# Optimization experiments

Measured on AMD Instinct MI355X. Metric: run time of the kernel, lower is better.

## Reference

```python
import jax, jax.numpy as jnp
import numpy as np

B, T, D, H, O = 128, 1024, 256, 512, 256

def setup_inputs() -> dict:
    key = jax.random.key(0)
    k0, k1, k2, k3 = jax.random.split(key, 4)
    s_i = 1.0 / np.sqrt(D)
    s_h = 1.0 / np.sqrt(H)
    return {
        "X": jax.random.normal(k0, (B, T, D), jnp.float32),
        "Wi": jax.random.normal(k1, (D, 4 * H), jnp.float32) * s_i,  # input kernel (no bias in flax OptimizedLSTMCell input dense)
        "Wh": jax.random.normal(k2, (H, 4 * H), jnp.float32) * s_h,  # recurrent kernel
        "b": jnp.zeros((4 * H,), jnp.float32),                        # recurrent bias
        "Wd": jax.random.normal(k3, (H, O), jnp.float32) * s_h,      # output Dense kernel
        "bd": jnp.zeros((O,), jnp.float32),                           # output Dense bias
    }

def _lstm_last_hidden(X, Wi, Wh, b):
    # Precompute input projections for all timesteps (same linear map, hoisted out of scan)
    x_proj = jnp.einsum('btd,dg->btg', X, Wi)  # [B, T, 4H]
    h_dim = Wh.shape[0]
    c0 = jnp.zeros((X.shape[0], h_dim), X.dtype)
    h0 = c0

    def step(carry, xt):
        c, h = carry
        y = xt + h @ Wh + b  # [B, 4H]
        i, f, g, o = jnp.split(y, 4, axis=-1)  # flax OptimizedLSTMCell gate order: i, f, g, o
        i = jax.nn.sigmoid(i)
        f = jax.nn.sigmoid(f)
        g = jnp.tanh(g)
        o = jax.nn.sigmoid(o)
        c_new = f * c + i * g
        h_new = o * jnp.tanh(c_new)
        return (c_new, h_new), None

    (c_T, h_T), _ = jax.lax.scan(step, (c0, h0), jnp.swapaxes(x_proj, 0, 1))
    return h_T  # [B, H] = last hidden state

def reference(X, Wi, Wh, b, Wd, bd):
    # Original applies Dense to all timesteps then slices [:, -1, :];
    # Dense is pointwise over time, so applying it to the last hidden is identical math.
    h_last = _lstm_last_hidden(X, Wi, Wh, b)
    return h_last @ Wd + bd  # [B, O]
```

## Files before the change

kernel.cpp:

```cpp
#include <hip/hip_runtime.h>
#include <hip/hip_bf16.h>

#define Bb 128
#define Tt 1024
#define Dd 256
#define Hh 512
#define G4 2048
#define Oo 256

#define NBG 8
#define WPB 8
#define NWG 64
#define BLOCK 512

#define SPIN_CAP (1u << 22)

typedef __attribute__((ext_vector_type(8)))  short  short8;
typedef __attribute__((ext_vector_type(4)))  float  f32x4;
typedef unsigned long long u64;

#define XCC_OFF  0
#define CNT_OFF  256
#define HBUF_OFF 4096
#define WS_ZERO_BYTES (4096 + Bb*Hh*2)

__device__ __forceinline__ short f2bf(float f) {
  __hip_bfloat16 h = __float2bfloat16(f);
  return *reinterpret_cast<short*>(&h);
}
__device__ __forceinline__ float sigm(float x) {
  return __builtin_amdgcn_rcpf(1.f + __expf(-x));
}
__device__ __forceinline__ float tanh_(float x) {
  return fmaf(2.f, __builtin_amdgcn_rcpf(1.f + __expf(-2.f * x)), -1.f);
}

__global__ __launch_bounds__(BLOCK, 2) void lstm_seq(
    const float* __restrict__ X, const float* __restrict__ Wi,
    const float* __restrict__ Wh, const float* __restrict__ bias,
    char* hbuf, int* cnts, int* xcc_post)
{
  __shared__ char sH[16 * 1024];
  __shared__ char sX[16 * 512];
  __shared__ float sY[8][16][36];
  __shared__ unsigned short hstage[16][72];
  __shared__ int sFast;

  const int tid  = threadIdx.x;
  const int w    = tid >> 6;
  const int lane = tid & 63;

  const int bg  = blockIdx.x & 7;
  const int gjw = blockIdx.x >> 3;

  int myxcc;
  asm volatile("s_getreg_b32 %0, hwreg(HW_REG_XCC_ID)" : "=s"(myxcc));
  if (tid == 0) {
    __hip_atomic_store(&xcc_post[blockIdx.x], myxcc + 1,
                       __ATOMIC_RELAXED, __HIP_MEMORY_SCOPE_AGENT);
    int ok = 1;
    for (int p = 0; p < WPB; ++p) {
      int v; unsigned spin = 0;
      do {
        v = __hip_atomic_load(&xcc_post[bg + p * NBG],
                              __ATOMIC_RELAXED, __HIP_MEMORY_SCOPE_AGENT);
      } while (v == 0 && ++spin < SPIN_CAP);
      ok &= (v == myxcc + 1);
    }
    sFast = ok;
  }
  __syncthreads();
  const bool fast = (sFast != 0);
  int* cnt = cnts + bg * 32;

  short8 wf[2][24];
  float bv[2];
#pragma unroll
  for (int nt = 0; nt < 2; ++nt) {
    int c = nt * 16 + (lane & 15);
    int gate = c >> 3, jj = c & 7;
    int colg = gate * Hh + gjw * 64 + w * 8 + jj;
    bv[nt] = bias[colg];
#pragma unroll
    for (int kk = 0; kk < 24; ++kk) {
      short8 f;
#pragma unroll
      for (int i = 0; i < 8; ++i) {
        int k = kk * 32 + (lane >> 4) * 8 + i;
        float v = (k < Hh) ? Wh[(size_t)k * G4 + colg]
                           : Wi[(size_t)(k - Hh) * G4 + colg];
        f[i] = f2bf(v);
      }
      wf[nt][kk] = f;
    }
  }

  const int ejj = lane & 7;
  const int er0 = lane >> 3;
  float cpr[2] = {0.f, 0.f};

  const int arow = lane & 15;
  const int kgrp = lane >> 4;
  const int aswz = (arow & 7) << 4;

  for (int s = 1; s <= Tt; ++s) {
    const char* hread  = hbuf + (size_t)((s - 1) & 1) * (Bb * Hh * 2);
    char*       hwrite = hbuf + (size_t)(s & 1) * (Bb * Hh * 2);

    {
      int row = tid >> 5, seg = tid & 31;
      const float* xp = X + ((size_t)(bg * 16 + row) * Tt + (s - 1)) * Dd + seg * 8;
      f32x4 x0 = *reinterpret_cast<const f32x4*>(xp);
      f32x4 x1 = *reinterpret_cast<const f32x4*>(xp + 4);
      short8 xb;
      xb[0] = f2bf(x0[0]); xb[1] = f2bf(x0[1]); xb[2] = f2bf(x0[2]); xb[3] = f2bf(x0[3]);
      xb[4] = f2bf(x1[0]); xb[5] = f2bf(x1[1]); xb[6] = f2bf(x1[2]); xb[7] = f2bf(x1[3]);
      *reinterpret_cast<short8*>(sX + row * 512 + ((seg * 16) ^ ((row & 7) << 4))) = xb;
    }

    if (s > 1 && tid == 0) {
      const int tgt = WPB * (s - 1);
      unsigned spin = 0;
      if (fast) {
        while ((__hip_atomic_fetch_add(cnt, 0x10000, __ATOMIC_RELAXED,
                                       __HIP_MEMORY_SCOPE_WORKGROUP) & 0xFFFF) < tgt
               && ++spin < SPIN_CAP) {
          __builtin_amdgcn_s_sleep(1);
        }
      } else {
        while (__hip_atomic_load(cnt, __ATOMIC_RELAXED,
                                 __HIP_MEMORY_SCOPE_AGENT) < tgt
               && ++spin < SPIN_CAP) {
          __builtin_amdgcn_s_sleep(1);
        }
      }
    }
    __syncthreads();

    if (fast) {
      asm volatile("buffer_inv sc0" ::: "memory");
#pragma unroll
      for (int q = 0; q < 2; ++q) {
        int c = tid + q * 512, row = c >> 6, off = c & 63;
        f32x4 v = *reinterpret_cast<const f32x4*>(
            hread + (size_t)(bg * 16 + row) * 1024 + off * 16);
        *reinterpret_cast<f32x4*>(sH + row * 1024 + ((off * 16) ^ ((row & 7) << 4))) = v;
      }
    } else {
#pragma unroll
      for (int q = 0; q < 2; ++q) {
        int c = tid + q * 512, row = c >> 6, off = c & 63;
        const u64* src = reinterpret_cast<const u64*>(
            hread + (size_t)(bg * 16 + row) * 1024 + off * 16);
        u64 lo = __hip_atomic_load(src,     __ATOMIC_RELAXED, __HIP_MEMORY_SCOPE_AGENT);
        u64 hi = __hip_atomic_load(src + 1, __ATOMIC_RELAXED, __HIP_MEMORY_SCOPE_AGENT);
        union { u64 u[2]; f32x4 v; } cv; cv.u[0] = lo; cv.u[1] = hi;
        *reinterpret_cast<f32x4*>(sH + row * 1024 + ((off * 16) ^ ((row & 7) << 4))) = cv.v;
      }
    }
    __syncthreads();

    f32x4 acc0, acc1;
#pragma unroll
    for (int m = 0; m < 4; ++m) { acc0[m] = bv[0]; acc1[m] = bv[1]; }
#pragma unroll
    for (int kk = 0; kk < 16; ++kk) {
      short8 a = *reinterpret_cast<const short8*>(
          sH + arow * 1024 + ((kk * 64 + kgrp * 16) ^ aswz));
      acc0 = __builtin_amdgcn_mfma_f32_16x16x32_bf16(a, wf[0][kk], acc0, 0, 0, 0);
      acc1 = __builtin_amdgcn_mfma_f32_16x16x32_bf16(a, wf[1][kk], acc1, 0, 0, 0);
    }
#pragma unroll
    for (int kk = 0; kk < 8; ++kk) {
      short8 a = *reinterpret_cast<const short8*>(
          sX + arow * 512 + ((kk * 64 + kgrp * 16) ^ aswz));
      acc0 = __builtin_amdgcn_mfma_f32_16x16x32_bf16(a, wf[0][16 + kk], acc0, 0, 0, 0);
      acc1 = __builtin_amdgcn_mfma_f32_16x16x32_bf16(a, wf[1][16 + kk], acc1, 0, 0, 0);
    }

    float* sYw = &sY[w][0][0];
#pragma unroll
    for (int m = 0; m < 4; ++m) {
      int row = kgrp * 4 + m;
      sYw[row * 36 + (lane & 15)]      = acc0[m];
      sYw[row * 36 + 16 + (lane & 15)] = acc1[m];
    }
#pragma unroll
    for (int q = 0; q < 2; ++q) {
      int r = er0 + q * 8;
      float yi = sYw[r * 36 + ejj];
      float yf = sYw[r * 36 + 8 + ejj];
      float yg = sYw[r * 36 + 16 + ejj];
      float yo = sYw[r * 36 + 24 + ejj];
      float ig = sigm(yi), fg = sigm(yf), gg = tanh_(yg), og = sigm(yo);
      float c = fg * cpr[q] + ig * gg;
      cpr[q] = c;
      float hh = og * tanh_(c);
      __hip_bfloat16 hb = __float2bfloat16(hh);
      hstage[r][w * 8 + ejj] = *reinterpret_cast<unsigned short*>(&hb);
    }
    __syncthreads();

    if (tid < 128) {
      int row = tid >> 3, colq = tid & 7;
      f32x4 v = *reinterpret_cast<const f32x4*>(
          reinterpret_cast<const char*>(&hstage[0][0]) + row * 144 + colq * 16);
      char* dst = hwrite + ((size_t)(bg * 16 + row) * Hh + gjw * 64 + colq * 8) * 2;
      if (fast) {
        *reinterpret_cast<f32x4*>(dst) = v;
      } else {
        union { f32x4 v; u64 u[2]; } cv; cv.v = v;
        u64* d64 = reinterpret_cast<u64*>(dst);
        __hip_atomic_store(d64,     cv.u[0], __ATOMIC_RELAXED, __HIP_MEMORY_SCOPE_AGENT);
        __hip_atomic_store(d64 + 1, cv.u[1], __ATOMIC_RELAXED, __HIP_MEMORY_SCOPE_AGENT);
      }
    }
    __syncthreads();

    if (tid == 0) {
      if (fast) (void)__hip_atomic_fetch_add(cnt, 1, __ATOMIC_RELAXED,
                                             __HIP_MEMORY_SCOPE_WORKGROUP);
      else      (void)__hip_atomic_fetch_add(cnt, 1, __ATOMIC_RELAXED,
                                             __HIP_MEMORY_SCOPE_AGENT);
    }
  }
}

__global__ void out_dense(const __hip_bfloat16* __restrict__ hT,
                          const float* __restrict__ Wd,
                          const float* __restrict__ bd,
                          float* __restrict__ out)
{
  __shared__ float hrow[Hh];
  int b = blockIdx.x;
  int o = threadIdx.x;
  for (int k = o; k < Hh; k += Oo)
    hrow[k] = __bfloat162float(hT[(size_t)b * Hh + k]);
  __syncthreads();
  float acc = bd[o];
  for (int k = 0; k < Hh; ++k)
    acc = fmaf(hrow[k], Wd[(size_t)k * Oo + o], acc);
  out[(size_t)b * Oo + o] = acc;
}

extern "C" void kernel_launch(void* const* d_in, const int* in_sizes, int n_in,
                              void* d_out, int out_size, void* d_ws, size_t ws_size,
                              hipStream_t stream) {
  (void)in_sizes; (void)n_in; (void)out_size; (void)ws_size;
  const float* X  = (const float*)d_in[0];
  const float* Wi = (const float*)d_in[1];
  const float* Wh = (const float*)d_in[2];
  const float* b  = (const float*)d_in[3];
  const float* Wd = (const float*)d_in[4];
  const float* bd = (const float*)d_in[5];
  float* out = (float*)d_out;

  char* ws = (char*)d_ws;
  int* xcc_post = (int*)(ws + XCC_OFF);
  int* cnts     = (int*)(ws + CNT_OFF);
  char* hbuf    = ws + HBUF_OFF;

  hipMemsetAsync(d_ws, 0, WS_ZERO_BYTES, stream);
  lstm_seq<<<NWG, BLOCK, 0, stream>>>(X, Wi, Wh, b, hbuf, cnts, xcc_post);
  out_dense<<<Bb, Oo, 0, stream>>>((const __hip_bfloat16*)hbuf, Wd, bd, out);
}
```

Measured before the change: 2.751 ms.

## Restructure LSTM step: direct global h loads, shuffle gate exchange, prefetch X, fewer barriers

Reworks the per-timestep schedule of the persistent LSTM kernel. X for the next steps is prefetched into registers two steps ahead, and its MFMA contribution is computed before the inter-block wait. On the fast path, h is loaded straight from global memory into MFMA operands instead of being staged through LDS. Gate values are exchanged with lane shuffles rather than an LDS round trip. h is written directly to global memory, and __syncthreads is replaced by raw s_barrier with explicit waitcnts. The spin-wait sleep is also removed. The changes aim to cut barriers and LDS traffic on the serial critical path, at the cost of uncoalesced 2-byte global stores and fragile manual memory ordering.

Result: slower. 8.194 ms (+197.8%).

```diff
diff --git a/kernel.cpp b/kernel.cpp
--- a/kernel.cpp
+++ b/kernel.cpp
@@ -34,6 +34,21 @@
 __device__ __forceinline__ float tanh_(float x) {
   return fmaf(2.f, __builtin_amdgcn_rcpf(1.f + __expf(-2.f * x)), -1.f);
 }
+
+__device__ __forceinline__ void bar_ctrl() {
+  asm volatile("s_barrier" ::: "memory");
+}
+__device__ __forceinline__ void bar_lds() {
+  asm volatile("s_waitcnt lgkmcnt(0)\n\ts_barrier" ::: "memory");
+}
+__device__ __forceinline__ void bar_vm2() {
+  asm volatile("s_waitcnt vmcnt(2) lgkmcnt(0)\n\ts_barrier" ::: "memory");
+}
+__device__ __forceinline__ void bar_vm0() {
+  asm volatile("s_waitcnt vmcnt(0) lgkmcnt(0)\n\ts_barrier" ::: "memory");
+}
+
+#define MFMA16(A, B, C) __builtin_amdgcn_mfma_f32_16x16x32_bf16((A), (B), (C), 0, 0, 0)
 
 __global__ __launch_bounds__(BLOCK, 2) void lstm_seq(
     const float* __restrict__ X, const float* __restrict__ Wi,
@@ -42,8 +57,6 @@
 {
   __shared__ char sH[16 * 1024];
   __shared__ char sX[16 * 512];
-  __shared__ float sY[8][16][36];
-  __shared__ unsigned short hstage[16][72];
   __shared__ int sFast;
 
   const int tid  = threadIdx.x;
@@ -78,8 +91,8 @@
 #pragma unroll
   for (int nt = 0; nt < 2; ++nt) {
     int c = nt * 16 + (lane & 15);
-    int gate = c >> 3, jj = c & 7;
-    int colg = gate * Hh + gjw * 64 + w * 8 + jj;
+    int gate = c >> 3, jj0 = c & 7;
+    int colg = gate * Hh + gjw * 64 + w * 8 + jj0;
     bv[nt] = bias[colg];
 #pragma unroll
     for (int kk = 0; kk < 24; ++kk) {
@@ -95,27 +108,43 @@
     }
   }
 
-  const int ejj = lane & 7;
-  const int er0 = lane >> 3;
+  const int cjj  = lane & 15;
+  const int kgrp = lane >> 4;
+  const int arow = cjj;
+  const int aswz = (arow & 7) << 4;
+  const int hi8  = (cjj >> 3) & 1;
+  const int jj   = cjj & 7;
+  const int ocol = gjw * 64 + w * 8 + jj;
   float cpr[2] = {0.f, 0.f};
 
-  const int arow = lane & 15;
-  const int kgrp = lane >> 4;
-  const int aswz = (arow & 7) << 4;
-
-  for (int s = 1; s <= Tt; ++s) {
-    const char* hread  = hbuf + (size_t)((s - 1) & 1) * (Bb * Hh * 2);
-    char*       hwrite = hbuf + (size_t)(s & 1) * (Bb * Hh * 2);
+  const int xrow = tid >> 5, xseg = tid & 31;
+  const float* xbase = X + (size_t)(bg * 16 + xrow) * Tt * Dd + xseg * 8;
+  f32x4 xA0 = *reinterpret_cast<const f32x4*>(xbase);
+  f32x4 xA1 = *reinterpret_cast<const f32x4*>(xbase + 4);
+  f32x4 xB0 = *reinterpret_cast<const f32x4*>(xbase + Dd);
+  f32x4 xB1 = *reinterpret_cast<const f32x4*>(xbase + Dd + 4);
+
+  auto STEP = [&](int s, f32x4& xv0, f32x4& xv1) {
+    const char* hread = hbuf + (size_t)((s - 1) & 1) * (Bb * Hh * 2);
+    char*      hwrite = hbuf + (size_t)(s & 1) * (Bb * Hh * 2);
 
     {
-      int row = tid >> 5, seg = tid & 31;
-      const float* xp = X + ((size_t)(bg * 16 + row) * Tt + (s - 1)) * Dd + seg * 8;
-      f32x4 x0 = *reinterpret_cast<const f32x4*>(xp);
-      f32x4 x1 = *reinterpret_cast<const f32x4*>(xp + 4);
       short8 xb;
-      xb[0] = f2bf(x0[0]); xb[1] = f2bf(x0[1]); xb[2] = f2bf(x0[2]); xb[3] = f2bf(x0[3]);
-      xb[4] = f2bf(x1[0]); xb[5] = f2bf(x1[1]); xb[6] = f2bf(x1[2]); xb[7] = f2bf(x1[3]);
-      *reinterpret_cast<short8*>(sX + row * 512 + ((seg * 16) ^ ((row & 7) << 4))) = xb;
+      xb[0] = f2bf(xv0[0]); xb[1] = f2bf(xv0[1]); xb[2] = f2bf(xv0[2]); xb[3] = f2bf(xv0[3]);
+      xb[4] = f2bf(xv1[0]); xb[5] = f2bf(xv1[1]); xb[6] = f2bf(xv1[2]); xb[7] = f2bf(xv1[3]);
+      *reinterpret_cast<short8*>(sX + xrow * 512 + ((xseg * 16) ^ ((xrow & 7) << 4))) = xb;
+    }
+    bar_lds();
+
+    f32x4 acc0, acc1;
+#pragma unroll
+    for (int m = 0; m < 4; ++m) { acc0[m] = bv[0]; acc1[m] = bv[1]; }
+#pragma unroll
+    for (int kk = 0; kk < 8; ++kk) {
+      short8 a = *reinterpret_cast<const short8*>(
+          sX + arow * 512 + ((kk * 64 + kgrp * 16) ^ aswz));
+      acc0 = MFMA16(a, wf[0][16 + kk], acc0);
+      acc1 = MFMA16(a, wf[1][16 + kk], acc1);
     }
 
     if (s > 1 && tid == 0) {
@@ -124,9 +153,7 @@
       if (fast) {
         while ((__hip_atomic_fetch_add(cnt, 0x10000, __ATOMIC_RELAXED,
                                        __HIP_MEMORY_SCOPE_WORKGROUP) & 0xFFFF) < tgt
-               && ++spin < SPIN_CAP) {
-          __builtin_amdgcn_s_sleep(1);
-        }
+               && ++spin < SPIN_CAP) {}
       } else {
         while (__hip_atomic_load(cnt, __ATOMIC_RELAXED,
                                  __HIP_MEMORY_SCOPE_AGENT) < tgt
@@ -135,17 +162,44 @@
         }
       }
     }
-    __syncthreads();
+    bar_ctrl();
 
     if (fast) {
       asm volatile("buffer_inv sc0" ::: "memory");
-#pragma unroll
-      for (int q = 0; q < 2; ++q) {
-        int c = tid + q * 512, row = c >> 6, off = c & 63;
-        f32x4 v = *reinterpret_cast<const f32x4*>(
-            hread + (size_t)(bg * 16 + row) * 1024 + off * 16);
-        *reinterpret_cast<f32x4*>(sH + row * 1024 + ((off * 16) ^ ((row & 7) << 4))) = v;
-      }
+      const char* hb = hread + (size_t)(bg * 16 + arow) * (Hh * 2) + kgrp * 16;
+      short8 a0, a1, a2, a3, b0, b1, b2, b3;
+      a0 = *reinterpret_cast<const short8*>(hb + 0 * 64);
+      a1 = *reinterpret_cast<const short8*>(hb + 1 * 64);
+      a2 = *reinterpret_cast<const short8*>(hb + 2 * 64);
+      a3 = *reinterpret_cast<const short8*>(hb + 3 * 64);
+      b0 = *reinterpret_cast<const short8*>(hb + 4 * 64);
+      b1 = *reinterpret_cast<const short8*>(hb + 5 * 64);
+      b2 = *reinterpret_cast<const short8*>(hb + 6 * 64);
+      b3 = *reinterpret_cast<const short8*>(hb + 7 * 64);
+      acc0 = MFMA16(a0, wf[0][0], acc0); acc1 = MFMA16(a0, wf[1][0], acc1);
+      acc0 = MFMA16(a1, wf[0][1], acc0); acc1 = MFMA16(a1, wf[1][1], acc1);
+      acc0 = MFMA16(a2, wf[0][2], acc0); acc1 = MFMA16(a2, wf[1][2], acc1);
+      acc0 = MFMA16(a3, wf[0][3], acc0); acc1 = MFMA16(a3, wf[1][3], acc1);
+      a0 = *reinterpret_cast<const short8*>(hb + 8 * 64);
+      a1 = *reinterpret_cast<const short8*>(hb + 9 * 64);
+      a2 = *reinterpret_cast<const short8*>(hb + 10 * 64);
+      a3 = *reinterpret_cast<const short8*>(hb + 11 * 64);
+      acc0 = MFMA16(b0, wf[0][4], acc0); acc1 = MFMA16(b0, wf[1][4], acc1);
+      acc0 = MFMA16(b1, wf[0][5], acc0); acc1 = MFMA16(b1, wf[1][5], acc1);
+      acc0 = MFMA16(b2, wf[0][6], acc0); acc1 = MFMA16(b2, wf[1][6], acc1);
+      acc0 = MFMA16(b3, wf[0][7], acc0); acc1 = MFMA16(b3, wf[1][7], acc1);
+      b0 = *reinterpret_cast<const short8*>(hb + 12 * 64);
+      b1 = *reinterpret_cast<const short8*>(hb + 13 * 64);
+      b2 = *reinterpret_cast<const short8*>(hb + 14 * 64);
+      b3 = *reinterpret_cast<const short8*>(hb + 15 * 64);
+      acc0 = MFMA16(a0, wf[0][8],  acc0); acc1 = MFMA16(a0, wf[1][8],  acc1);
+      acc0 = MFMA16(a1, wf[0][9],  acc0); acc1 = MFMA16(a1, wf[1][9],  acc1);
+      acc0 = MFMA16(a2, wf[0][10], acc0); acc1 = MFMA16(a2, wf[1][10], acc1);
+      acc0 = MFMA16(a3, wf[0][11], acc0); acc1 = MFMA16(a3, wf[1][11], acc1);
+      acc0 = MFMA16(b0, wf[0][12], acc0); acc1 = MFMA16(b0, wf[1][12], acc1);
+      acc0 = MFMA16(b1, wf[0][13], acc0); acc1 = MFMA16(b1, wf[1][13], acc1);
+      acc0 = MFMA16(b2, wf[0][14], acc0); acc1 = MFMA16(b2, wf[1][14], acc1);
+      acc0 = MFMA16(b3, wf[0][15], acc0); acc1 = MFMA16(b3, wf[1][15], acc1);
     } else {
 #pragma unroll
       for (int q = 0; q < 2; ++q) {
@@ -157,65 +211,67 @@
         union { u64 u[2]; f32x4 v; } cv; cv.u[0] = lo; cv.u[1] = hi;
         *reinterpret_cast<f32x4*>(sH + row * 1024 + ((off * 16) ^ ((row & 7) << 4))) = cv.v;
       }
-    }
-    __syncthreads();
-
-    f32x4 acc0, acc1;
-#pragma unroll
-    for (int m = 0; m < 4; ++m) { acc0[m] = bv[0]; acc1[m] = bv[1]; }
-#pragma unroll
-    for (int kk = 0; kk < 16; ++kk) {
-      short8 a = *reinterpret_cast<const short8*>(
-          sH + arow * 1024 + ((kk * 64 + kgrp * 16) ^ aswz));
-      acc0 = __builtin_amdgcn_mfma_f32_16x16x32_bf16(a, wf[0][kk], acc0, 0, 0, 0);
-      acc1 = __builtin_amdgcn_mfma_f32_16x16x32_bf16(a, wf[1][kk], acc1, 0, 0, 0);
-    }
-#pragma unroll
-    for (int kk = 0; kk < 8; ++kk) {
-      short8 a = *reinterpret_cast<const short8*>(
-          sX + arow * 512 + ((kk * 64 + kgrp * 16) ^ aswz));
-      acc0 = __builtin_amdgcn_mfma_f32_16x16x32_bf16(a, wf[0][16 + kk], acc0, 0, 0, 0);
-      acc1 = __builtin_amdgcn_mfma_f32_16x16x32_bf16(a, wf[1][16 + kk], acc1, 0, 0, 0);
-    }
-
-    float* sYw = &sY[w][0][0];
+      bar_lds();
+#pragma unroll
+      for (int kk = 0; kk < 16; ++kk) {
+        short8 a = *reinterpret_cast<const short8*>(
+            sH + arow * 1024 + ((kk * 64 + kgrp * 16) ^ aswz));
+        acc0 = MFMA16(a, wf[0][kk], acc0);
+        acc1 = MFMA16(a, wf[1][kk], acc1);
+      }
+    }
+
+    float o0[4], o1[4];
 #pragma unroll
     for (int m = 0; m < 4; ++m) {
-      int row = kgrp * 4 + m;
-      sYw[row * 36 + (lane & 15)]      = acc0[m];
-      sYw[row * 36 + 16 + (lane & 15)] = acc1[m];
-    }
+      o0[m] = __shfl_xor(acc0[m], 8);
+      o1[m] = __shfl_xor(acc1[m], 8);
+    }
+    float hv[2];
 #pragma unroll
     for (int q = 0; q < 2; ++q) {
-      int r = er0 + q * 8;
-      float yi = sYw[r * 36 + ejj];
-      float yf = sYw[r * 36 + 8 + ejj];
-      float yg = sYw[r * 36 + 16 + ejj];
-      float yo = sYw[r * 36 + 24 + ejj];
-      float ig = sigm(yi), fg = sigm(yf), gg = tanh_(yg), og = sigm(yo);
+      int m = hi8 * 2 + q;
+      float iv = hi8 ? o0[m]   : acc0[m];
+      float fv = hi8 ? acc0[m] : o0[m];
+      float gv = hi8 ? o1[m]   : acc1[m];
+      float ov = hi8 ? acc1[m] : o1[m];
+      float ig = sigm(iv), fg = sigm(fv), gg = tanh_(gv), og = sigm(ov);
       float c = fg * cpr[q] + ig * gg;
       cpr[q] = c;
-      float hh = og * tanh_(c);
-      __hip_bfloat16 hb = __float2bfloat16(hh);
-      hstage[r][w * 8 + ejj] = *reinterpret_cast<unsigned short*>(&hb);
-    }
-    __syncthreads();
-
-    if (tid < 128) {
-      int row = tid >> 3, colq = tid & 7;
-      f32x4 v = *reinterpret_cast<const f32x4*>(
-          reinterpret_cast<const char*>(&hstage[0][0]) + row * 144 + colq * 16);
-      char* dst = hwrite + ((size_t)(bg * 16 + row) * Hh + gjw * 64 + colq * 8) * 2;
-      if (fast) {
-        *reinterpret_cast<f32x4*>(dst) = v;
-      } else {
-        union { f32x4 v; u64 u[2]; } cv; cv.v = v;
-        u64* d64 = reinterpret_cast<u64*>(dst);
+      hv[q] = og * tanh_(c);
+    }
+    const int orow = kgrp * 4 + hi8 * 2;
+
+    if (fast) {
+      __hip_bfloat16* hw = reinterpret_cast<__hip_bfloat16*>(hwrite)
+                           + (size_t)(bg * 16 + orow) * Hh + ocol;
+      hw[0]  = __float2bfloat16(hv[0]);
+      hw[Hh] = __float2bfloat16(hv[1]);
+    } else {
+      unsigned short* hs = reinterpret_cast<unsigned short*>(sX);
+      __hip_bfloat16 h0 = __float2bfloat16(hv[0]), h1 = __float2bfloat16(hv[1]);
+      hs[orow * 72 + w * 8 + jj]       = *reinterpret_cast<unsigned short*>(&h0);
+      hs[(orow + 1) * 72 + w * 8 + jj] = *reinterpret_cast<unsigned short*>(&h1);
+      bar_lds();
+      if (tid < 128) {
+        int row = tid >> 3, colq = tid & 7;
+        union { f32x4 v; u64 u[2]; } cv;
+        cv.v = *reinterpret_cast<const f32x4*>(
+            reinterpret_cast<const char*>(hs) + row * 144 + colq * 16);
+        u64* d64 = reinterpret_cast<u64*>(
+            hwrite + ((size_t)(bg * 16 + row) * Hh + gjw * 64 + colq * 8) * 2);
         __hip_atomic_store(d64,     cv.u[0], __ATOMIC_RELAXED, __HIP_MEMORY_SCOPE_AGENT);
         __hip_atomic_store(d64 + 1, cv.u[1], __ATOMIC_RELAXED, __HIP_MEMORY_SCOPE_AGENT);
       }
     }
-    __syncthreads();
+
+    if (s + 2 <= Tt) {
+      xv0 = *reinterpret_cast<const f32x4*>(xbase + (size_t)(s + 1) * Dd);
+      xv1 = *reinterpret_cast<const f32x4*>(xbase + (size_t)(s + 1) * Dd + 4);
+      bar_vm2();
+    } else {
+      bar_vm0();
+    }
 
     if (tid == 0) {
       if (fast) (void)__hip_atomic_fetch_add(cnt, 1, __ATOMIC_RELAXED,
@@ -223,6 +279,11 @@
       else      (void)__hip_atomic_fetch_add(cnt, 1, __ATOMIC_RELAXED,
                                              __HIP_MEMORY_SCOPE_AGENT);
     }
+  };
+
+  for (int s = 1; s <= Tt; s += 2) {
+    STEP(s,     xA0, xA1);
+    STEP(s + 1, xB0, xB1);
   }
 }
 
```
